# Kernel optimization log

Measured on AMD Instinct MI355X. Metric: run time of the kernel, lower is better.

Reference implementation:

```python
import jax, jax.numpy as jnp
import numpy as np

B, P, H, K, IN_DIM, OUT_DIM = 256, 512, 16, 8, 4, 1


def setup_inputs() -> dict:
    key = jax.random.key(0)
    ks = jax.random.split(key, 16)
    s = lambda k, shp, scale: (jax.random.normal(k, shp, dtype=jnp.float32) * scale)
    inp = {
        "x_pf": jax.random.normal(ks[0], (B * P, IN_DIM), dtype=jnp.float32),
        "batch_pf": jnp.repeat(jnp.arange(B, dtype=jnp.int64 if jax.config.jax_enable_x64 else jnp.int32), P),
        "num_graphs": B,
        # pf_encode: Linear(4,16), Linear(16,16)
        "W_e1": s(ks[1], (IN_DIM, H), 0.5), "b_e1": s(ks[2], (H,), 0.1),
        "W_e2": s(ks[3], (H, H), 0.25), "b_e2": s(ks[4], (H,), 0.1),
        # DynamicEdgeConv nn: Linear(2H, H)
        "W_c": s(ks[5], (2 * H, H), 0.2), "b_c": s(ks[6], (H,), 0.1),
        # output head: Linear(16,8), Linear(8,4), Linear(4,1)
        "W_o1": s(ks[7], (H, 8), 0.25), "b_o1": s(ks[8], (8,), 0.1),
        "W_o2": s(ks[9], (8, 4), 0.35), "b_o2": s(ks[10], (4,), 0.1),
        "W_o3": s(ks[11], (4, OUT_DIM), 0.5), "b_o3": s(ks[12], (OUT_DIM,), 0.1),
    }
    return inp


def _edgeconv(h, W_c, b_c, n_graphs):
    # h: [N, H]; graphs are contiguous blocks of equal size P (batch_pf = repeat(arange(B), P))
    p = h.shape[0] // n_graphs
    hb = h.reshape(n_graphs, p, h.shape[-1])              # [B, P, H]
    sq = jnp.sum(hb * hb, axis=-1)                        # [B, P]
    # pairwise squared distances per graph: [B, P, P]
    d2 = sq[:, :, None] + sq[:, None, :] - 2.0 * jnp.einsum("bpd,bqd->bpq", hb, hb)
    _, idx = jax.lax.top_k(-d2, K)                        # k nearest (incl. self), [B, P, k]
    xj = jnp.take_along_axis(hb[:, None, :, :], idx[:, :, :, None], axis=2)  # [B, P, k, H]
    xi = hb[:, :, None, :]                                # [B, P, 1, H]
    e = jnp.concatenate([jnp.broadcast_to(xi, xj.shape), xj - xi], axis=-1)  # [B, P, k, 2H]
    m = jax.nn.elu(e @ W_c + b_c)                         # edge MLP
    return jnp.max(m, axis=2).reshape(h.shape[0], -1)     # max aggregation -> [N, H]


def _forward(x_pf, W_e1, b_e1, W_e2, b_e2, W_c, b_c, W_o1, b_o1, W_o2, b_o2, W_o3, b_o3, n_graphs):
    elu = jax.nn.elu
    h = elu(elu(x_pf @ W_e1 + b_e1) @ W_e2 + b_e2)        # pf_encode, [N, H]
    f1 = _edgeconv(h, W_c, b_c, n_graphs)                 # DynamicEdgeConv (same weights both calls)
    f2 = _edgeconv(f1, W_c, b_c, n_graphs)
    p = f2.shape[0] // n_graphs
    pooled = f2.reshape(n_graphs, p, -1).mean(axis=1)     # avg_pool_x over batch -> [B, H]
    out = elu(pooled @ W_o1 + b_o1)
    out = elu(out @ W_o2 + b_o2)
    out = out @ W_o3 + b_o3                               # [B, 1]
    return out


def reference(x_pf, batch_pf, num_graphs, W_e1, b_e1, W_e2, b_e2, W_c, b_c,
              W_o1, b_o1, W_o2, b_o2, W_o3, b_o3):
    out = _forward(x_pf, W_e1, b_e1, W_e2, b_e2, W_c, b_c,
                   W_o1, b_o1, W_o2, b_o2, W_o3, b_o3, int(num_graphs))
    pooled_batch = jnp.arange(int(num_graphs), dtype=batch_pf.dtype)
    return out, pooled_batch
```

## Files before the change

### kernel.cpp

```cpp
#include <hip/hip_runtime.h>
#include <math.h>

#define NB 256
#define NP 512
#define NH 16
#define NK 8

__device__ __forceinline__ float elu_f(float x) { return x > 0.0f ? x : expm1f(x); }

__global__ __launch_bounds__(256) void k_encoder(
    const float* __restrict__ x,
    const float* __restrict__ We1, const float* __restrict__ be1,
    const float* __restrict__ We2, const float* __restrict__ be2,
    float* __restrict__ h, float* __restrict__ sq)
{
    int i = blockIdx.x * 256 + threadIdx.x;
    float4 xv = reinterpret_cast<const float4*>(x)[i];
    float h1[NH];
#pragma unroll
    for (int o = 0; o < NH; ++o) {
        float a = be1[o];
        a = fmaf(xv.x, We1[0*NH+o], a);
        a = fmaf(xv.y, We1[1*NH+o], a);
        a = fmaf(xv.z, We1[2*NH+o], a);
        a = fmaf(xv.w, We1[3*NH+o], a);
        h1[o] = elu_f(a);
    }
    float hv[NH];
    float s = 0.0f;
#pragma unroll
    for (int o = 0; o < NH; ++o) {
        float a = be2[o];
#pragma unroll
        for (int q = 0; q < NH; ++q) a = fmaf(h1[q], We2[q*NH+o], a);
        a = elu_f(a);
        hv[o] = a;
        s = fmaf(a, a, s);
    }
#pragma unroll
    for (int d = 0; d < NH; d += 4)
        *reinterpret_cast<float4*>(h + (size_t)i*NH + d) =
            make_float4(hv[d], hv[d+1], hv[d+2], hv[d+3]);
    sq[i] = s;
}

template<int FINAL>
__global__ __launch_bounds__(512) void k_conv(
    const float* __restrict__ hin, const float* __restrict__ sqin,
    const float* __restrict__ Wc, const float* __restrict__ bc,
    float* hout, float* sqout,
    const float* __restrict__ Wo1, const float* __restrict__ bo1,
    const float* __restrict__ Wo2, const float* __restrict__ bo2,
    const float* __restrict__ Wo3, const float* __restrict__ bo3,
    float* __restrict__ out)
{
    __shared__ float hs[NP * NH];
    __shared__ float sqs[NP];

    const int g = blockIdx.x;
    const int t = threadIdx.x;

    float xi[NH];
    {
        const float4* hg4 = reinterpret_cast<const float4*>(hin + (size_t)g * NP * NH);
        float4* hs4 = reinterpret_cast<float4*>(hs);
#pragma unroll
        for (int d4 = 0; d4 < 4; ++d4) {
            float4 v = hg4[(size_t)t * 4 + d4];
            hs4[t * 4 + d4] = v;
            xi[d4*4+0] = v.x; xi[d4*4+1] = v.y; xi[d4*4+2] = v.z; xi[d4*4+3] = v.w;
        }
    }
    const float sqi = sqin[(size_t)g * NP + t];
    sqs[t] = sqi;
    __syncthreads();

    float bd[NK]; int bj[NK];
#pragma unroll
    for (int k = 0; k < NK; ++k) { bd[k] = 3.402823466e38f; bj[k] = 0; }

#pragma unroll 4
    for (int j = 0; j < NP; ++j) {
        const float* row = hs + j * NH;
        float dot = 0.0f;
#pragma unroll
        for (int d = 0; d < NH; ++d) dot = fmaf(row[d], xi[d], dot);
        float d2 = sqi + sqs[j] - 2.0f * dot;
        if (d2 < bd[NK-1]) {
            float dc = d2; int jc = j;
#pragma unroll
            for (int k = 0; k < NK; ++k) {
                if (dc < bd[k]) {
                    float td = bd[k]; int tj = bj[k];
                    bd[k] = dc; bj[k] = jc; dc = td; jc = tj;
                }
            }
        }
    }

    float base[NH];
#pragma unroll
    for (int o = 0; o < NH; ++o) base[o] = bc[o];
#pragma unroll
    for (int d = 0; d < NH; ++d) {
        float xv = xi[d];
#pragma unroll
        for (int o = 0; o < NH; ++o) base[o] = fmaf(xv, Wc[d*NH+o], base[o]);
    }

    float f[NH];
#pragma unroll
    for (int o = 0; o < NH; ++o) f[o] = -3.402823466e38f;
#pragma unroll
    for (int k = 0; k < NK; ++k) {
        const float* rj = hs + bj[k] * NH;
        float m[NH];
#pragma unroll
        for (int o = 0; o < NH; ++o) m[o] = base[o];
#pragma unroll
        for (int d = 0; d < NH; ++d) {
            float dx = rj[d] - xi[d];
#pragma unroll
            for (int o = 0; o < NH; ++o) m[o] = fmaf(dx, Wc[(NH+d)*NH+o], m[o]);
        }
#pragma unroll
        for (int o = 0; o < NH; ++o) f[o] = fmaxf(f[o], elu_f(m[o]));
    }

    if (FINAL == 0) {
        float s = 0.0f;
#pragma unroll
        for (int d = 0; d < NH; ++d) s = fmaf(f[d], f[d], s);
#pragma unroll
        for (int d = 0; d < NH; d += 4)
            *reinterpret_cast<float4*>(hout + (size_t)(g * NP + t) * NH + d) =
                make_float4(f[d], f[d+1], f[d+2], f[d+3]);
        sqout[(size_t)g * NP + t] = s;
    } else {
        __shared__ float red[8][NH];
#pragma unroll
        for (int d = 0; d < NH; ++d) {
            float v = f[d];
            v += __shfl_down(v, 32);
            v += __shfl_down(v, 16);
            v += __shfl_down(v, 8);
            v += __shfl_down(v, 4);
            v += __shfl_down(v, 2);
            v += __shfl_down(v, 1);
            f[d] = v;
        }
        const int lane = t & 63, w = t >> 6;
        if (lane == 0) {
#pragma unroll
            for (int d = 0; d < NH; ++d) red[w][d] = f[d];
        }
        __syncthreads();
        if (t == 0) {
            float pooled[NH];
#pragma unroll
            for (int d = 0; d < NH; ++d) {
                float s = red[0][d];
#pragma unroll
                for (int w2 = 1; w2 < 8; ++w2) s += red[w2][d];
                pooled[d] = s * (1.0f/512.0f);
            }
            float o1[8];
#pragma unroll
            for (int o = 0; o < 8; ++o) {
                float a = bo1[o];
#pragma unroll
                for (int q = 0; q < NH; ++q) a = fmaf(pooled[q], Wo1[q*8+o], a);
                o1[o] = elu_f(a);
            }
            float o2[4];
#pragma unroll
            for (int o = 0; o < 4; ++o) {
                float a = bo2[o];
#pragma unroll
                for (int q = 0; q < 8; ++q) a = fmaf(o1[q], Wo2[q*4+o], a);
                o2[o] = elu_f(a);
            }
            float r = bo3[0];
#pragma unroll
            for (int q = 0; q < 4; ++q) r = fmaf(o2[q], Wo3[q], r);
            out[g] = r;
            out[NB + g] = (float)g;
        }
    }
}

extern "C" void kernel_launch(void* const* d_in, const int* in_sizes, int n_in,
                              void* d_out, int out_size, void* d_ws, size_t ws_size,
                              hipStream_t stream)
{
    const float* x   = (const float*)d_in[0];
    const float* We1 = (const float*)d_in[3];
    const float* be1 = (const float*)d_in[4];
    const float* We2 = (const float*)d_in[5];
    const float* be2 = (const float*)d_in[6];
    const float* Wc  = (const float*)d_in[7];
    const float* bc  = (const float*)d_in[8];
    const float* Wo1 = (const float*)d_in[9];
    const float* bo1 = (const float*)d_in[10];
    const float* Wo2 = (const float*)d_in[11];
    const float* bo2 = (const float*)d_in[12];
    const float* Wo3 = (const float*)d_in[13];
    const float* bo3 = (const float*)d_in[14];
    float* out = (float*)d_out;

    const size_t NPTS = (size_t)NB * NP;
    float* h   = (float*)d_ws;
    float* sq0 = h + NPTS*NH;
    float* f1;
    float* sq1;
    const size_t need = (NPTS*NH + NPTS) * 2 * sizeof(float);
    if (ws_size >= need) {
        f1  = sq0 + NPTS;
        sq1 = f1 + NPTS*NH;
    } else {
        f1  = h;
        sq1 = sq0;
    }

    k_encoder<<<dim3((unsigned)(NPTS/256)), dim3(256), 0, stream>>>(
        x, We1, be1, We2, be2, h, sq0);
    k_conv<0><<<dim3(NB), dim3(512), 0, stream>>>(
        h, sq0, Wc, bc, f1, sq1,
        nullptr, nullptr, nullptr, nullptr, nullptr, nullptr, nullptr);
    k_conv<1><<<dim3(NB), dim3(512), 0, stream>>>(
        f1, sq1, Wc, bc, nullptr, nullptr,
        Wo1, bo1, Wo2, bo2, Wo3, bo3, out);
}
```

Before: 607.3 us.

## Split kNN candidate scan across two threads per point and merge via shared memory

Each graph block now uses 1024 threads, with two threads per point. Each thread scans half of the 512 candidates for top-k, and the two partial lists are merged through shared memory. The edge-MLP work is also split, each half handling 4 of the 8 neighbors, and the max results are combined through shared memory. This doubles the threads available to the serial O(P) distance scan on 256 blocks, which would otherwise underfill the GPU. In exchange it adds roughly 80KB of shared memory, extra syncs and merge work, and may limit occupancy or register budget.

```diff
diff --git a/kernel.cpp b/kernel.cpp
--- a/kernel.cpp
+++ b/kernel.cpp
@@ -45,7 +45,7 @@
 }
 
 template<int FINAL>
-__global__ __launch_bounds__(512) void k_conv(
+__global__ __launch_bounds__(1024, 4) void k_conv(
     const float* __restrict__ hin, const float* __restrict__ sqin,
     const float* __restrict__ Wc, const float* __restrict__ bc,
     float* hout, float* sqout,
@@ -56,31 +56,37 @@
 {
     __shared__ float hs[NP * NH];
     __shared__ float sqs[NP];
+    __shared__ float pbd[NP * NK];
+    __shared__ int   pbj[NP * NK];
+    __shared__ float fbuf[NP * NH];
 
     const int g = blockIdx.x;
     const int t = threadIdx.x;
-
-    float xi[NH];
-    {
+    const int p = t & (NP - 1);
+    const int half = t >> 9;
+    const int jb = half * (NP / 2);
+
+    if (t < NP) {
         const float4* hg4 = reinterpret_cast<const float4*>(hin + (size_t)g * NP * NH);
         float4* hs4 = reinterpret_cast<float4*>(hs);
 #pragma unroll
-        for (int d4 = 0; d4 < 4; ++d4) {
-            float4 v = hg4[(size_t)t * 4 + d4];
-            hs4[t * 4 + d4] = v;
-            xi[d4*4+0] = v.x; xi[d4*4+1] = v.y; xi[d4*4+2] = v.z; xi[d4*4+3] = v.w;
-        }
-    }
-    const float sqi = sqin[(size_t)g * NP + t];
-    sqs[t] = sqi;
-    __syncthreads();
+        for (int d4 = 0; d4 < 4; ++d4) hs4[t * 4 + d4] = hg4[(size_t)t * 4 + d4];
+        sqs[t] = sqin[(size_t)g * NP + t];
+    }
+    __syncthreads();
+
+    float xi[NH];
+#pragma unroll
+    for (int d = 0; d < NH; ++d) xi[d] = hs[p * NH + d];
+    const float sqi = sqs[p];
 
     float bd[NK]; int bj[NK];
 #pragma unroll
     for (int k = 0; k < NK; ++k) { bd[k] = 3.402823466e38f; bj[k] = 0; }
 
 #pragma unroll 4
-    for (int j = 0; j < NP; ++j) {
+    for (int jo = 0; jo < NP / 2; ++jo) {
+        const int j = jb + jo;
         const float* row = hs + j * NH;
         float dot = 0.0f;
 #pragma unroll
@@ -98,6 +104,40 @@
         }
     }
 
+    if (half) {
+#pragma unroll
+        for (int k = 0; k < NK; ++k) { pbd[p*NK+k] = bd[k]; pbj[p*NK+k] = bj[k]; }
+    }
+    __syncthreads();
+
+    if (!half) {
+#pragma unroll
+        for (int k2 = 0; k2 < NK; ++k2) {
+            float dc = pbd[p*NK+k2]; int jc = pbj[p*NK+k2];
+            if (dc < bd[NK-1]) {
+#pragma unroll
+                for (int k = 0; k < NK; ++k) {
+                    if (dc < bd[k]) {
+                        float td = bd[k]; int tj = bj[k];
+                        bd[k] = dc; bj[k] = jc; dc = td; jc = tj;
+                    }
+                }
+            }
+        }
+#pragma unroll
+        for (int k = 4; k < NK; ++k) pbj[p*NK+k] = bj[k];
+    }
+    __syncthreads();
+
+    int ej[4];
+    if (!half) {
+#pragma unroll
+        for (int c = 0; c < 4; ++c) ej[c] = bj[c];
+    } else {
+#pragma unroll
+        for (int c = 0; c < 4; ++c) ej[c] = pbj[p*NK+4+c];
+    }
+
     float base[NH];
 #pragma unroll
     for (int o = 0; o < NH; ++o) base[o] = bc[o];
@@ -112,8 +152,8 @@
 #pragma unroll
     for (int o = 0; o < NH; ++o) f[o] = -3.402823466e38f;
 #pragma unroll
-    for (int k = 0; k < NK; ++k) {
-        const float* rj = hs + bj[k] * NH;
+    for (int c = 0; c < 4; ++c) {
+        const float* rj = hs + ej[c] * NH;
         float m[NH];
 #pragma unroll
         for (int o = 0; o < NH; ++o) m[o] = base[o];
@@ -127,32 +167,46 @@
         for (int o = 0; o < NH; ++o) f[o] = fmaxf(f[o], elu_f(m[o]));
     }
 
-    if (FINAL == 0) {
-        float s = 0.0f;
-#pragma unroll
-        for (int d = 0; d < NH; ++d) s = fmaf(f[d], f[d], s);
+    if (half) {
 #pragma unroll
         for (int d = 0; d < NH; d += 4)
-            *reinterpret_cast<float4*>(hout + (size_t)(g * NP + t) * NH + d) =
+            *reinterpret_cast<float4*>(fbuf + p*NH + d) =
                 make_float4(f[d], f[d+1], f[d+2], f[d+3]);
-        sqout[(size_t)g * NP + t] = s;
+    }
+    __syncthreads();
+
+    if constexpr (FINAL == 0) {
+        if (!half) {
+#pragma unroll
+            for (int d = 0; d < NH; ++d) f[d] = fmaxf(f[d], fbuf[p*NH+d]);
+            float s = 0.0f;
+#pragma unroll
+            for (int d = 0; d < NH; ++d) s = fmaf(f[d], f[d], s);
+#pragma unroll
+            for (int d = 0; d < NH; d += 4)
+                *reinterpret_cast<float4*>(hout + (size_t)(g * NP + p) * NH + d) =
+                    make_float4(f[d], f[d+1], f[d+2], f[d+3]);
+            sqout[(size_t)g * NP + p] = s;
+        }
     } else {
         __shared__ float red[8][NH];
-#pragma unroll
-        for (int d = 0; d < NH; ++d) {
-            float v = f[d];
-            v += __shfl_down(v, 32);
-            v += __shfl_down(v, 16);
-            v += __shfl_down(v, 8);
-            v += __shfl_down(v, 4);
-            v += __shfl_down(v, 2);
-            v += __shfl_down(v, 1);
-            f[d] = v;
-        }
-        const int lane = t & 63, w = t >> 6;
-        if (lane == 0) {
-#pragma unroll
-            for (int d = 0; d < NH; ++d) red[w][d] = f[d];
+        if (!half) {
+#pragma unroll
+            for (int d = 0; d < NH; ++d) {
+                float v = fmaxf(f[d], fbuf[p*NH+d]);
+                v += __shfl_down(v, 32);
+                v += __shfl_down(v, 16);
+                v += __shfl_down(v, 8);
+                v += __shfl_down(v, 4);
+                v += __shfl_down(v, 2);
+                v += __shfl_down(v, 1);
+                f[d] = v;
+            }
+            const int lane = t & 63, w = t >> 6;
+            if (lane == 0) {
+#pragma unroll
+                for (int d = 0; d < NH; ++d) red[w][d] = f[d];
+            }
         }
         __syncthreads();
         if (t == 0) {
@@ -224,10 +278,10 @@
 
     k_encoder<<<dim3((unsigned)(NPTS/256)), dim3(256), 0, stream>>>(
         x, We1, be1, We2, be2, h, sq0);
-    k_conv<0><<<dim3(NB), dim3(512), 0, stream>>>(
+    k_conv<0><<<dim3(NB), dim3(1024), 0, stream>>>(
         h, sq0, Wc, bc, f1, sq1,
         nullptr, nullptr, nullptr, nullptr, nullptr, nullptr, nullptr);
-    k_conv<1><<<dim3(NB), dim3(512), 0, stream>>>(
+    k_conv<1><<<dim3(NB), dim3(1024), 0, stream>>>(
         f1, sq1, Wc, bc, nullptr, nullptr,
         Wo1, bo1, Wo2, bo2, Wo3, bo3, out);
 }
```

After: 875.6 us. +44.2%, slower.
